# Kernel optimization log

Hardware: AMD Instinct MI355X
Metric: run time of the kernel (lower is better)

The kernel has to match this reference:

```python
import jax, jax.numpy as jnp
import numpy as np

EMBED_DIM = 512
NUM_HEADS = 8
HEAD_DIM = EMBED_DIM // NUM_HEADS


def setup_inputs() -> dict:
    key = jax.random.key(0)
    ks = jax.random.split(key, 12)
    B, T, S, E = 4, 1024, 1024, EMBED_DIM
    inp = {
        "queries": jax.random.normal(ks[0], (B, T, E), dtype=jnp.float32),
        "keys": jax.random.normal(ks[1], (B, S, E), dtype=jnp.float32),
        "values": jax.random.normal(ks[2], (B, S, E), dtype=jnp.float32),
        # Linear weights stored torch-style: (out_features, in_features)
        "Wq": jax.random.normal(ks[3], (E, E), dtype=jnp.float32) * 0.02,
        "bq": jnp.zeros((E,), dtype=jnp.float32),
        "Wk": jax.random.normal(ks[4], (E, E), dtype=jnp.float32) * 0.02,
        "bk": jnp.zeros((E,), dtype=jnp.float32),
        "Wv": jax.random.normal(ks[5], (E, E), dtype=jnp.float32) * 0.02,
        "bv": jnp.zeros((E,), dtype=jnp.float32),
        "Wo": jax.random.normal(ks[6], (E, E), dtype=jnp.float32) * 0.02,
        "bo": jnp.zeros((E,), dtype=jnp.float32),
        # True = padding; all False -> no padding (keeps softmax rows finite)
        "q_padding_mask": jnp.zeros((B, T), dtype=bool),
        "key_padding_mask": jnp.zeros((B, S), dtype=bool),
        # True = attendable; all True
        "attn_mask": jnp.ones((T, S), dtype=bool),
    }
    return inp


def _split_heads(x):
    # (B, L, E) -> (B, H, L, head_dim)
    B, L, E = x.shape
    return x.reshape(B, L, NUM_HEADS, HEAD_DIM).transpose(0, 2, 1, 3)


def reference(queries, keys, values, Wq, bq, Wk, bk, Wv, bv, Wo, bo,
              q_padding_mask, key_padding_mask, attn_mask):
    B, T, E = queries.shape
    # input projections
    q = queries @ Wq.T + bq
    k = keys @ Wk.T + bk
    v = values @ Wv.T + bv
    q = _split_heads(q)  # (B,H,T,hd)
    k = _split_heads(k)  # (B,H,S,hd)
    v = _split_heads(v)  # (B,H,S,hd)
    # compute_scores: scaled dot-product
    scores = jnp.einsum('bhtd,bhsd->bhts', q, k) / jnp.sqrt(
        jnp.asarray(HEAD_DIM, dtype=q.dtype))
    neg_inf = jnp.asarray(-jnp.inf, dtype=scores.dtype)
    # key padding: True -> masked out
    scores = jnp.where(key_padding_mask[:, None, None, :], neg_inf, scores)
    # attn_mask: True -> attendable
    scores = jnp.where(~attn_mask[None, None, :, :], neg_inf, scores)
    weights = jax.nn.softmax(scores, axis=-1)  # (B,H,T,S)
    # zero out padded query rows
    weights = jnp.where(q_padding_mask[:, None, :, None],
                        jnp.asarray(0.0, weights.dtype), weights)
    ctx = jnp.einsum('bhts,bhsd->bhtd', weights, v)  # (B,H,T,hd)
    ctx = ctx.transpose(0, 2, 1, 3).reshape(B, T, E)
    out = ctx @ Wo.T + bo
    return out
```

## Files before the change

### kernel.cpp

```cpp
#include <hip/hip_runtime.h>
#include <math.h>

#define EDIM 512
#define HEADS 8
#define HD 64
#define BATCH 4
#define SEQ 1024
#define MROWS (BATCH*SEQ)
#define LOG2E 1.44269504088896340736f

typedef _Float16 half8 __attribute__((ext_vector_type(8)));
typedef _Float16 half4 __attribute__((ext_vector_type(4)));
typedef __fp16 fp16x2 __attribute__((ext_vector_type(2)));
typedef float f32x4 __attribute__((ext_vector_type(4)));

#define MFMA16(a, b, c) __builtin_amdgcn_mfma_f32_16x16x32_f16((a), (b), (c), 0, 0, 0)

__device__ __forceinline__ void gload16(const void* g, void* l) {
    __builtin_amdgcn_global_load_lds(
        (const __attribute__((address_space(1))) unsigned int*)g,
        (__attribute__((address_space(3))) unsigned int*)l, 16, 0, 0);
}

__global__ __launch_bounds__(512, 4)
void gemm_qkv(const float* __restrict__ Xq, const float* __restrict__ Xk,
              const float* __restrict__ Xv,
              const float* __restrict__ Wq, const float* __restrict__ Wk,
              const float* __restrict__ Wv,
              const float* __restrict__ bq, const float* __restrict__ bk,
              const float* __restrict__ bv, _Float16* __restrict__ Yb)
{
    __shared__ _Float16 As[2][128 * 64];
    __shared__ _Float16 Bs[2][128 * 64];

    const int tid  = threadIdx.x;
    const int lane = tid & 63;
    const int q16  = lane & 15;
    const int g    = lane >> 4;
    const int wid  = tid >> 6;
    const int wm   = wid >> 2, wn = wid & 3;
    const int id    = blockIdx.x;
    const int n0    = (id / 96) * 128;
    const int mw    = id % 96;
    const int which = mw >> 5;
    const int m0    = (mw & 31) * 128;
    const size_t BIG = (size_t)MROWS * EDIM;

    const float* X = which == 0 ? Xq : which == 1 ? Xk : Xv;
    const float* W = which == 0 ? Wq : which == 1 ? Wk : Wv;
    const float* bias = which == 0 ? bq : which == 1 ? bk : bv;
    _Float16* Y = Yb + (size_t)which * BIG;
    const float oscale = which == 0 ? (0.125f * LOG2E) : 1.0f;

    const int xr = tid >> 2;
    const int xc = (tid & 3) * 4;

    f32x4 acc[4][2];
    #pragma unroll
    for (int i = 0; i < 4; ++i)
        #pragma unroll
        for (int j = 0; j < 2; ++j) acc[i][j] = (f32x4){0.f,0.f,0.f,0.f};

    auto stage = [&](const float* S, int srow0, int koff, _Float16* dstBuf) {
        #pragma unroll
        for (int i = 0; i < 4; ++i) {
            const int c = xc + i * 16;
            const float4 x = *(const float4*)
                &S[(size_t)(srow0 + xr) * EDIM + koff + c];
            half4 hh;
            hh[0] = (_Float16)x.x; hh[1] = (_Float16)x.y;
            hh[2] = (_Float16)x.z; hh[3] = (_Float16)x.w;
            *(half4*)&dstBuf[xr * 64 + (((c >> 3) ^ (xr & 7)) << 3) + (c & 7)] = hh;
        }
    };

    stage(X, m0, 0, &As[0][0]);
    stage(W, n0, 0, &Bs[0][0]);
    __syncthreads();

    for (int kt = 0; kt < 8; ++kt) {
        const int cur = kt & 1;
        float4 xv[4], wv[4];
        if (kt < 7) {
            const int koff = (kt + 1) * 64;
            #pragma unroll
            for (int i = 0; i < 4; ++i) {
                xv[i] = *(const float4*)
                    &X[(size_t)(m0 + xr) * EDIM + koff + xc + i * 16];
                wv[i] = *(const float4*)
                    &W[(size_t)(n0 + xr) * EDIM + koff + xc + i * 16];
            }
        }
        #pragma unroll
        for (int ks = 0; ks < 2; ++ks) {
            const int gr = 4 * ks + g;
            half8 a[4], b[2];
            #pragma unroll
            for (int mf = 0; mf < 4; ++mf) {
                const int row = wm * 64 + mf * 16 + q16;
                a[mf] = *(const half8*)&As[cur][row * 64 + ((gr ^ (row & 7)) << 3)];
            }
            #pragma unroll
            for (int nf = 0; nf < 2; ++nf) {
                const int row = wn * 32 + nf * 16 + q16;
                b[nf] = *(const half8*)&Bs[cur][row * 64 + ((gr ^ (row & 7)) << 3)];
            }
            #pragma unroll
            for (int mf = 0; mf < 4; ++mf)
                #pragma unroll
                for (int nf = 0; nf < 2; ++nf)
                    acc[mf][nf] = MFMA16(a[mf], b[nf], acc[mf][nf]);
        }
        if (kt < 7) {
            #pragma unroll
            for (int i = 0; i < 4; ++i) {
                const int c = xc + i * 16;
                half4 ha, hb;
                ha[0] = (_Float16)xv[i].x; ha[1] = (_Float16)xv[i].y;
                ha[2] = (_Float16)xv[i].z; ha[3] = (_Float16)xv[i].w;
                hb[0] = (_Float16)wv[i].x; hb[1] = (_Float16)wv[i].y;
                hb[2] = (_Float16)wv[i].z; hb[3] = (_Float16)wv[i].w;
                const int off = xr * 64 + (((c >> 3) ^ (xr & 7)) << 3) + (c & 7);
                *(half4*)&As[cur ^ 1][off] = ha;
                *(half4*)&Bs[cur ^ 1][off] = hb;
            }
        }
        __syncthreads();
    }

    if (which < 2) {
        #pragma unroll
        for (int mf = 0; mf < 4; ++mf)
            #pragma unroll
            for (int nf = 0; nf < 2; ++nf) {
                const int col = n0 + wn * 32 + nf * 16 + q16;
                const float bvv = bias[col];
                #pragma unroll
                for (int r = 0; r < 4; ++r) {
                    const int rowg = m0 + wm * 64 + mf * 16 + g * 4 + r;
                    Y[(size_t)rowg * EDIM + col] =
                        (_Float16)((acc[mf][nf][r] + bvv) * oscale);
                }
            }
    } else {
        #pragma unroll
        for (int mf = 0; mf < 4; ++mf) {
            const int tok = m0 + wm * 64 + mf * 16 + g * 4;
            const int b2  = tok >> 10;
            const int ts  = tok & 1023;
            const int so  = ts & 63;
            const int sp2 = 32 * (so >> 5) + 8 * ((so >> 2) & 3) + 4 * ((so >> 4) & 1);
            const size_t scol = (size_t)(ts & ~63) + sp2;
            #pragma unroll
            for (int nf = 0; nf < 2; ++nf) {
                const int col = n0 + wn * 32 + nf * 16 + q16;
                const float bvv = bias[col];
                const int hh2 = col >> 6, dd = col & 63;
                half4 hv;
                hv[0] = (_Float16)(acc[mf][nf][0] + bvv);
                hv[1] = (_Float16)(acc[mf][nf][1] + bvv);
                hv[2] = (_Float16)(acc[mf][nf][2] + bvv);
                hv[3] = (_Float16)(acc[mf][nf][3] + bvv);
                *(half4*)&Y[(size_t)((b2 * 8 + hh2) * 64 + dd) * SEQ + scol] = hv;
            }
        }
    }
}

__global__ __launch_bounds__(256)
void attn16(const _Float16* __restrict__ Qg, const _Float16* __restrict__ Kg,
            const _Float16* __restrict__ Vt, _Float16* __restrict__ Cp,
            float* __restrict__ scal)
{
    __shared__ _Float16 Ks[2][64 * 64];
    __shared__ _Float16 Vs[2][64 * 64];

    const int tid  = threadIdx.x;
    const int lane = tid & 63;
    const int w    = tid >> 6;
    const int g    = lane >> 4;
    const int q16  = lane & 15;
    const int id   = blockIdx.x;
    const int qt   = id >> 6;
    const int rem  = id & 63;
    const int sp   = rem >> 5;
    const int bh   = rem & 31;
    const int b    = bh >> 3, h = bh & 7;
    const size_t qbase = ((size_t)b * SEQ + qt * 64) * EDIM + h * 64;
    const size_t kbase = ((size_t)b * SEQ + sp * (SEQ / 2)) * EDIM + h * 64;
    const size_t vbase = ((size_t)(b * 8 + h) * 64) * SEQ + sp * (SEQ / 2);
    const int NT = SEQ / 128;

    const int c0 = tid, c1 = tid + 256;
    const int row0 = c0 >> 3, row1 = c1 >> 3;
    const size_t gsrc0 = (size_t)row0 * EDIM + ((c0 & 7) ^ (row0 & 7)) * 8;
    const size_t gsrc1 = (size_t)row1 * EDIM + ((c1 & 7) ^ (row1 & 7)) * 8;
    const size_t vsrc0 = (size_t)row0 * SEQ + ((c0 & 7) ^ (row0 & 7)) * 8;
    const size_t vsrc1 = (size_t)row1 * SEQ + ((c1 & 7) ^ (row1 & 7)) * 8;

    gload16(&Qg[qbase + gsrc0], &Ks[0][c0 * 8]);
    gload16(&Qg[qbase + gsrc1], &Ks[0][c1 * 8]);
    __syncthreads();
    half8 aq[2];
    {
        const int row = w * 16 + q16;
        #pragma unroll
        for (int ks = 0; ks < 2; ++ks) {
            const int col = ks * 32 + g * 8;
            aq[ks] = *(const half8*)&Ks[0][row * 64 + (col ^ ((row & 7) << 3))];
        }
    }
    __syncthreads();

    gload16(&Kg[kbase + gsrc0], &Ks[0][c0 * 8]);
    gload16(&Kg[kbase + gsrc1], &Ks[0][c1 * 8]);
    gload16(&Vt[vbase + vsrc0], &Vs[0][c0 * 8]);
    gload16(&Vt[vbase + vsrc1], &Vs[0][c1 * 8]);
    __syncthreads();

    f32x4 o[4];
    #pragma unroll
    for (int mt = 0; mt < 4; ++mt) o[mt] = (f32x4){0.f,0.f,0.f,0.f};
    float m_run = -1e30f, l_run = 0.f;
    int cur = 0;

    for (int kt = 0; kt < NT; ++kt) {
        if (kt + 1 < NT) {
            const size_t nk = kbase + (size_t)((kt + 1) * 64) * EDIM;
            const size_t nv = vbase + (kt + 1) * 64;
            gload16(&Kg[nk + gsrc0], &Ks[cur ^ 1][c0 * 8]);
            gload16(&Kg[nk + gsrc1], &Ks[cur ^ 1][c1 * 8]);
            gload16(&Vt[nv + vsrc0], &Vs[cur ^ 1][c0 * 8]);
            gload16(&Vt[nv + vsrc1], &Vs[cur ^ 1][c1 * 8]);
        }

        f32x4 s4[4];
        #pragma unroll
        for (int mt = 0; mt < 4; ++mt) s4[mt] = (f32x4){0.f,0.f,0.f,0.f};
        __builtin_amdgcn_s_setprio(1);
        #pragma unroll
        for (int ks = 0; ks < 2; ++ks) {
            const int col = ks * 32 + g * 8;
            #pragma unroll
            for (int mt = 0; mt < 4; ++mt) {
                const int row = mt * 16 + q16;
                half8 kf = *(const half8*)&Ks[cur][row * 64 + (col ^ ((row & 7) << 3))];
                s4[mt] = MFMA16(kf, aq[ks], s4[mt]);
            }
        }
        __builtin_amdgcn_s_setprio(0);

        const float x0 = fmaxf(fmaxf(s4[0][0], s4[0][1]), fmaxf(s4[0][2], s4[0][3]));
        const float x1 = fmaxf(fmaxf(s4[1][0], s4[1][1]), fmaxf(s4[1][2], s4[1][3]));
        const float x2 = fmaxf(fmaxf(s4[2][0], s4[2][1]), fmaxf(s4[2][2], s4[2][3]));
        const float x3 = fmaxf(fmaxf(s4[3][0], s4[3][1]), fmaxf(s4[3][2], s4[3][3]));
        float pmax = fmaxf(fmaxf(x0, x1), fmaxf(x2, x3));
        pmax = fmaxf(pmax, __shfl_xor(pmax, 16));
        pmax = fmaxf(pmax, __shfl_xor(pmax, 32));
        if (!__all(pmax - m_run <= 11.f)) {
            const float mnew  = fmaxf(m_run, pmax);
            const float alpha = exp2f(m_run - mnew);
            #pragma unroll
            for (int mt = 0; mt < 4; ++mt) o[mt] *= alpha;
            l_run *= alpha;
            m_run = mnew;
        }
        #pragma unroll
        for (int mt = 0; mt < 4; ++mt)
            #pragma unroll
            for (int r = 0; r < 4; ++r)
                s4[mt][r] = exp2f(s4[mt][r] - m_run);
        const float r0 = (s4[0][0] + s4[0][1]) + (s4[0][2] + s4[0][3]);
        const float r1 = (s4[1][0] + s4[1][1]) + (s4[1][2] + s4[1][3]);
        const float r2 = (s4[2][0] + s4[2][1]) + (s4[2][2] + s4[2][3]);
        const float r3 = (s4[3][0] + s4[3][1]) + (s4[3][2] + s4[3][3]);
        float rs = (r0 + r1) + (r2 + r3);
        rs += __shfl_xor(rs, 16);
        rs += __shfl_xor(rs, 32);
        l_run += rs;

        half8 pf0, pf1;
        {
            union { half8 h8; fp16x2 h2[4]; } u0, u1;
            u0.h2[0] = __builtin_amdgcn_cvt_pkrtz(s4[0][0], s4[0][1]);
            u0.h2[1] = __builtin_amdgcn_cvt_pkrtz(s4[0][2], s4[0][3]);
            u0.h2[2] = __builtin_amdgcn_cvt_pkrtz(s4[1][0], s4[1][1]);
            u0.h2[3] = __builtin_amdgcn_cvt_pkrtz(s4[1][2], s4[1][3]);
            u1.h2[0] = __builtin_amdgcn_cvt_pkrtz(s4[2][0], s4[2][1]);
            u1.h2[1] = __builtin_amdgcn_cvt_pkrtz(s4[2][2], s4[2][3]);
            u1.h2[2] = __builtin_amdgcn_cvt_pkrtz(s4[3][0], s4[3][1]);
            u1.h2[3] = __builtin_amdgcn_cvt_pkrtz(s4[3][2], s4[3][3]);
            pf0 = u0.h8;
            pf1 = u1.h8;
        }

        __builtin_amdgcn_s_setprio(1);
        #pragma unroll
        for (int mtd = 0; mtd < 4; ++mtd) {
            const int row = mtd * 16 + q16;
            half8 vb0 = *(const half8*)&Vs[cur][row * 64 + (((g) ^ (row & 7)) << 3)];
            half8 vb1 = *(const half8*)&Vs[cur][row * 64 + (((g + 4) ^ (row & 7)) << 3)];
            o[mtd] = MFMA16(vb0, pf0, o[mtd]);
            o[mtd] = MFMA16(vb1, pf1, o[mtd]);
        }
        __builtin_amdgcn_s_setprio(0);

        __syncthreads();
        cur ^= 1;
    }

    const float inv  = 1.f / l_run;
    const int rowq   = qt * 64 + w * 16 + q16;
    const size_t grow = (size_t)b * SEQ + rowq;
    const size_t obase = grow * EDIM + h * 64;
    #pragma unroll
    for (int mtd = 0; mtd < 4; ++mtd) {
        half4 hv;
        hv[0] = (_Float16)(o[mtd][0] * inv);
        hv[1] = (_Float16)(o[mtd][1] * inv);
        hv[2] = (_Float16)(o[mtd][2] * inv);
        hv[3] = (_Float16)(o[mtd][3] * inv);
        *(half4*)&Cp[(size_t)sp * ((size_t)MROWS * EDIM) + obase + mtd * 16 + g * 4] = hv;
    }
    if (g == 0)
        scal[(size_t)sp * (MROWS * HEADS) + grow * HEADS + h] = m_run + log2f(l_run);
}

__global__ __launch_bounds__(256)
void gemm_oc(const _Float16* __restrict__ Cp, const float* __restrict__ scal,
             const float* __restrict__ W, const float* __restrict__ bias,
             float* __restrict__ Y)
{
    __shared__ _Float16 As[2][64 * 64];
    __shared__ _Float16 Bs[2][64 * 64];
    __shared__ float2   wgt[64 * 8];

    const int tid  = threadIdx.x;
    const int lane = tid & 63;
    const int q16  = lane & 15;
    const int g    = lane >> 4;
    const int wid  = tid >> 6;
    const int wm   = wid >> 1, wn = wid & 1;
    const int id   = blockIdx.x;
    const int n0   = (id >> 6) * 64;
    const int m0   = (id & 63) * 64;
    const size_t BIG = (size_t)MROWS * EDIM;

    {
        const int idx = tid * 2;
        #pragma unroll
        for (int i = 0; i < 2; ++i) {
            const int row = (idx + i) >> 3, h = (idx + i) & 7;
            const size_t grow = (size_t)m0 + row;
            const float s1 = scal[grow * HEADS + h];
            const float s2 = scal[(size_t)MROWS * HEADS + grow * HEADS + h];
            const float sm = fmaxf(s1, s2);
            const float w1 = exp2f(s1 - sm), w2 = exp2f(s2 - sm);
            const float dn = 1.f / (w1 + w2);
            wgt[idx + i] = (float2){w1 * dn, w2 * dn};
        }
    }

    const int arow = tid >> 2;
    const int ac4  = (tid & 3) * 4;
    const int ag8  = tid & 3;

    f32x4 acc[2][2];
    #pragma unroll
    for (int i = 0; i < 2; ++i)
        #pragma unroll
        for (int j = 0; j < 2; ++j) acc[i][j] = (f32x4){0.f,0.f,0.f,0.f};

    __syncthreads();

    auto stageA = [&](int kt, _Float16* dst) {
        #pragma unroll
        for (int i = 0; i < 2; ++i) {
            const int g8 = ag8 * 2 + i;
            const size_t src = (size_t)(m0 + arow) * EDIM + kt * 64 + g8 * 8;
            half8 x = *(const half8*)&Cp[src];
            half8 y = *(const half8*)&Cp[BIG + src];
            const float2 wt = wgt[arow * 8 + kt];
            half8 z;
            #pragma unroll
            for (int j = 0; j < 8; ++j)
                z[j] = (_Float16)(wt.x * (float)x[j] + wt.y * (float)y[j]);
            *(half8*)&dst[arow * 64 + ((g8 ^ (arow & 7)) << 3)] = z;
        }
    };
    auto stageB = [&](int kt, _Float16* dst) {
        #pragma unroll
        for (int i = 0; i < 4; ++i) {
            const int c = ac4 + i * 16;
            const float4 x = *(const float4*)
                &W[(size_t)(n0 + arow) * EDIM + kt * 64 + c];
            half4 hh;
            hh[0] = (_Float16)x.x; hh[1] = (_Float16)x.y;
            hh[2] = (_Float16)x.z; hh[3] = (_Float16)x.w;
            *(half4*)&dst[arow * 64 + (((c >> 3) ^ (arow & 7)) << 3) + (c & 7)] = hh;
        }
    };

    stageA(0, &As[0][0]);
    stageB(0, &Bs[0][0]);
    __syncthreads();

    for (int kt = 0; kt < 8; ++kt) {
        const int cur = kt & 1;
        half8 px[2], py[2];
        float4 wv4[4];
        if (kt < 7) {
            #pragma unroll
            for (int i = 0; i < 2; ++i) {
                const int g8 = ag8 * 2 + i;
                const size_t src = (size_t)(m0 + arow) * EDIM + (kt + 1) * 64 + g8 * 8;
                px[i] = *(const half8*)&Cp[src];
                py[i] = *(const half8*)&Cp[BIG + src];
            }
            #pragma unroll
            for (int i = 0; i < 4; ++i)
                wv4[i] = *(const float4*)
                    &W[(size_t)(n0 + arow) * EDIM + (kt + 1) * 64 + ac4 + i * 16];
        }
        #pragma unroll
        for (int ks = 0; ks < 2; ++ks) {
            const int gr = 4 * ks + g;
            half8 a[2], b[2];
            #pragma unroll
            for (int mf = 0; mf < 2; ++mf) {
                const int row = wm * 32 + mf * 16 + q16;
                a[mf] = *(const half8*)&As[cur][row * 64 + ((gr ^ (row & 7)) << 3)];
            }
            #pragma unroll
            for (int nf = 0; nf < 2; ++nf) {
                const int row = wn * 32 + nf * 16 + q16;
                b[nf] = *(const half8*)&Bs[cur][row * 64 + ((gr ^ (row & 7)) << 3)];
            }
            #pragma unroll
            for (int mf = 0; mf < 2; ++mf)
                #pragma unroll
                for (int nf = 0; nf < 2; ++nf)
                    acc[mf][nf] = MFMA16(a[mf], b[nf], acc[mf][nf]);
        }
        if (kt < 7) {
            const float2 wt = wgt[arow * 8 + kt + 1];
            #pragma unroll
            for (int i = 0; i < 2; ++i) {
                const int g8 = ag8 * 2 + i;
                half8 z;
                #pragma unroll
                for (int j = 0; j < 8; ++j)
                    z[j] = (_Float16)(wt.x * (float)px[i][j] + wt.y * (float)py[i][j]);
                *(half8*)&As[cur ^ 1][arow * 64 + ((g8 ^ (arow & 7)) << 3)] = z;
            }
            #pragma unroll
            for (int i = 0; i < 4; ++i) {
                const int c = ac4 + i * 16;
                half4 hh;
                hh[0] = (_Float16)wv4[i].x; hh[1] = (_Float16)wv4[i].y;
                hh[2] = (_Float16)wv4[i].z; hh[3] = (_Float16)wv4[i].w;
                *(half4*)&Bs[cur ^ 1][arow * 64 +
                    (((c >> 3) ^ (arow & 7)) << 3) + (c & 7)] = hh;
            }
        }
        __syncthreads();
    }

    #pragma unroll
    for (int mf = 0; mf < 2; ++mf)
        #pragma unroll
        for (int nf = 0; nf < 2; ++nf) {
            const int col = n0 + wn * 32 + nf * 16 + q16;
            const float bvv = bias[col];
            #pragma unroll
            for (int r = 0; r < 4; ++r) {
                const int rowg = m0 + wm * 32 + mf * 16 + g * 4 + r;
                Y[(size_t)rowg * EDIM + col] = acc[mf][nf][r] + bvv;
            }
        }
}

extern "C" void kernel_launch(void* const* d_in, const int* in_sizes, int n_in,
                              void* d_out, int out_size, void* d_ws, size_t ws_size,
                              hipStream_t stream) {
    const float* queries = (const float*)d_in[0];
    const float* keys    = (const float*)d_in[1];
    const float* values  = (const float*)d_in[2];
    const float* Wq = (const float*)d_in[3];
    const float* bq = (const float*)d_in[4];
    const float* Wk = (const float*)d_in[5];
    const float* bk = (const float*)d_in[6];
    const float* Wv = (const float*)d_in[7];
    const float* bv = (const float*)d_in[8];
    const float* Wo = (const float*)d_in[9];
    const float* bo = (const float*)d_in[10];
    float* out = (float*)d_out;

    const size_t BIG = (size_t)MROWS * EDIM;
    _Float16* f16ws = (_Float16*)d_ws;
    _Float16* Qb  = f16ws;
    _Float16* Kb  = Qb + BIG;
    _Float16* Vtg = Kb + BIG;
    _Float16* Cp  = Vtg + BIG;
    float*    scal = (float*)(Cp + 2 * BIG);

    gemm_qkv<<<dim3(384), dim3(512), 0, stream>>>(
        queries, keys, values, Wq, Wk, Wv, bq, bk, bv, Qb);

    attn16<<<dim3(1024), dim3(256), 0, stream>>>(
        Qb, Kb, Vtg, Cp, scal);

    gemm_oc<<<dim3(512), dim3(256), 0, stream>>>(
        Cp, scal, Wo, bo, out);
}
```

Baseline: 56.68 us.

## Split attention key dimension four ways and merge partials in output GEMM

Raises the flash-decoding style split of the key/value sequence from 2 to 4 chunks, doubling attention grid blocks to 2048 while halving the per-block loop length. The output projection kernel now reads four partial context tensors and four log-sum-exp scalars, combining them with softmax-style weights before the GEMM. This is meant to improve occupancy and load balance in attention. In exchange it doubles the partial-context write and read traffic and adds more per-block prologue overhead relative to work.

```diff
diff --git a/kernel.cpp b/kernel.cpp
--- a/kernel.cpp
+++ b/kernel.cpp
@@ -8,6 +8,7 @@
 #define SEQ 1024
 #define MROWS (BATCH*SEQ)
 #define LOG2E 1.44269504088896340736f
+#define NSPLIT 4
 
 typedef _Float16 half8 __attribute__((ext_vector_type(8)));
 typedef _Float16 half4 __attribute__((ext_vector_type(4)));
@@ -181,15 +182,15 @@
     const int g    = lane >> 4;
     const int q16  = lane & 15;
     const int id   = blockIdx.x;
-    const int qt   = id >> 6;
-    const int rem  = id & 63;
+    const int qt   = id >> 7;
+    const int rem  = id & 127;
     const int sp   = rem >> 5;
     const int bh   = rem & 31;
     const int b    = bh >> 3, h = bh & 7;
     const size_t qbase = ((size_t)b * SEQ + qt * 64) * EDIM + h * 64;
-    const size_t kbase = ((size_t)b * SEQ + sp * (SEQ / 2)) * EDIM + h * 64;
-    const size_t vbase = ((size_t)(b * 8 + h) * 64) * SEQ + sp * (SEQ / 2);
-    const int NT = SEQ / 128;
+    const size_t kbase = ((size_t)b * SEQ + sp * (SEQ / NSPLIT)) * EDIM + h * 64;
+    const size_t vbase = ((size_t)(b * 8 + h) * 64) * SEQ + sp * (SEQ / NSPLIT);
+    const int NT = SEQ / NSPLIT / 64;
 
     const int c0 = tid, c1 = tid + 256;
     const int row0 = c0 >> 3, row1 = c1 >> 3;
@@ -333,7 +334,7 @@
 {
     __shared__ _Float16 As[2][64 * 64];
     __shared__ _Float16 Bs[2][64 * 64];
-    __shared__ float2   wgt[64 * 8];
+    __shared__ float4   wgt[64 * 8];
 
     const int tid  = threadIdx.x;
     const int lane = tid & 63;
@@ -345,6 +346,7 @@
     const int n0   = (id >> 6) * 64;
     const int m0   = (id & 63) * 64;
     const size_t BIG = (size_t)MROWS * EDIM;
+    const size_t SSTR = (size_t)MROWS * HEADS;
 
     {
         const int idx = tid * 2;
@@ -353,11 +355,14 @@
             const int row = (idx + i) >> 3, h = (idx + i) & 7;
             const size_t grow = (size_t)m0 + row;
             const float s1 = scal[grow * HEADS + h];
-            const float s2 = scal[(size_t)MROWS * HEADS + grow * HEADS + h];
-            const float sm = fmaxf(s1, s2);
+            const float s2 = scal[SSTR + grow * HEADS + h];
+            const float s3 = scal[2 * SSTR + grow * HEADS + h];
+            const float s4v = scal[3 * SSTR + grow * HEADS + h];
+            const float sm = fmaxf(fmaxf(s1, s2), fmaxf(s3, s4v));
             const float w1 = exp2f(s1 - sm), w2 = exp2f(s2 - sm);
-            const float dn = 1.f / (w1 + w2);
-            wgt[idx + i] = (float2){w1 * dn, w2 * dn};
+            const float w3 = exp2f(s3 - sm), w4 = exp2f(s4v - sm);
+            const float dn = 1.f / ((w1 + w2) + (w3 + w4));
+            wgt[idx + i] = (float4){w1 * dn, w2 * dn, w3 * dn, w4 * dn};
         }
     }
 
@@ -378,13 +383,16 @@
         for (int i = 0; i < 2; ++i) {
             const int g8 = ag8 * 2 + i;
             const size_t src = (size_t)(m0 + arow) * EDIM + kt * 64 + g8 * 8;
-            half8 x = *(const half8*)&Cp[src];
-            half8 y = *(const half8*)&Cp[BIG + src];
-            const float2 wt = wgt[arow * 8 + kt];
+            half8 x1 = *(const half8*)&Cp[src];
+            half8 x2 = *(const half8*)&Cp[BIG + src];
+            half8 x3 = *(const half8*)&Cp[2 * BIG + src];
+            half8 x4 = *(const half8*)&Cp[3 * BIG + src];
+            const float4 wt = wgt[arow * 8 + kt];
             half8 z;
             #pragma unroll
             for (int j = 0; j < 8; ++j)
-                z[j] = (_Float16)(wt.x * (float)x[j] + wt.y * (float)y[j]);
+                z[j] = (_Float16)(((wt.x * (float)x1[j] + wt.y * (float)x2[j]) +
+                                   (wt.z * (float)x3[j] + wt.w * (float)x4[j])));
             *(half8*)&dst[arow * 64 + ((g8 ^ (arow & 7)) << 3)] = z;
         }
     };
@@ -407,15 +415,17 @@
 
     for (int kt = 0; kt < 8; ++kt) {
         const int cur = kt & 1;
-        half8 px[2], py[2];
+        half8 px[2][4];
         float4 wv4[4];
         if (kt < 7) {
             #pragma unroll
             for (int i = 0; i < 2; ++i) {
                 const int g8 = ag8 * 2 + i;
                 const size_t src = (size_t)(m0 + arow) * EDIM + (kt + 1) * 64 + g8 * 8;
-                px[i] = *(const half8*)&Cp[src];
-                py[i] = *(const half8*)&Cp[BIG + src];
+                px[i][0] = *(const half8*)&Cp[src];
+                px[i][1] = *(const half8*)&Cp[BIG + src];
+                px[i][2] = *(const half8*)&Cp[2 * BIG + src];
+                px[i][3] = *(const half8*)&Cp[3 * BIG + src];
             }
             #pragma unroll
             for (int i = 0; i < 4; ++i)
@@ -443,14 +453,15 @@
                     acc[mf][nf] = MFMA16(a[mf], b[nf], acc[mf][nf]);
         }
         if (kt < 7) {
-            const float2 wt = wgt[arow * 8 + kt + 1];
+            const float4 wt = wgt[arow * 8 + kt + 1];
             #pragma unroll
             for (int i = 0; i < 2; ++i) {
                 const int g8 = ag8 * 2 + i;
                 half8 z;
                 #pragma unroll
                 for (int j = 0; j < 8; ++j)
-                    z[j] = (_Float16)(wt.x * (float)px[i][j] + wt.y * (float)py[i][j]);
+                    z[j] = (_Float16)(((wt.x * (float)px[i][0][j] + wt.y * (float)px[i][1][j]) +
+                                       (wt.z * (float)px[i][2][j] + wt.w * (float)px[i][3][j])));
                 *(half8*)&As[cur ^ 1][arow * 64 + ((g8 ^ (arow & 7)) << 3)] = z;
             }
             #pragma unroll
@@ -502,12 +513,12 @@
     _Float16* Kb  = Qb + BIG;
     _Float16* Vtg = Kb + BIG;
     _Float16* Cp  = Vtg + BIG;
-    float*    scal = (float*)(Cp + 2 * BIG);
+    float*    scal = (float*)(Cp + NSPLIT * BIG);
 
     gemm_qkv<<<dim3(384), dim3(512), 0, stream>>>(
         queries, keys, values, Wq, Wk, Wv, bq, bk, bv, Qb);
 
-    attn16<<<dim3(1024), dim3(256), 0, stream>>>(
+    attn16<<<dim3(16 * 32 * NSPLIT), dim3(256), 0, stream>>>(
         Qb, Kb, Vtg, Cp, scal);
 
     gemm_oc<<<dim3(512), dim3(256), 0, stream>>>(
```

New measurement: 59.82 us. 5.5% more time.
